# Kernel tuning notes

Measured on AMD Instinct MI355X. Metric: run time of the kernel, lower is better.

Reference implementation:

```python
import jax, jax.numpy as jnp
import numpy as np

D_IN = 1024
D_OUT = 1024
SEQ = 4096


def setup_inputs() -> dict:
    key = jax.random.key(0)
    k0, k1, k2, k3 = jax.random.split(key, 4)
    inputs = jax.random.normal(k0, (SEQ, D_IN), dtype=jnp.float32)
    # original uses torch.rand (uniform [0,1)) for weights
    W_q = jax.random.uniform(k1, (D_IN, D_OUT), dtype=jnp.float32)
    W_k = jax.random.uniform(k2, (D_IN, D_OUT), dtype=jnp.float32)
    W_v = jax.random.uniform(k3, (D_IN, D_OUT), dtype=jnp.float32)
    return {"inputs": inputs, "W_q": W_q, "W_k": W_k, "W_v": W_v}


def reference(inputs, W_q, W_k, W_v):
    queries = inputs @ W_q            # [S, d_out]
    keys = inputs @ W_k               # [S, d_out]
    values = inputs @ W_v             # [S, d_out]
    d_k = keys.shape[-1]
    scale = 1.0 / jnp.sqrt(jnp.asarray(d_k, dtype=queries.dtype))
    attn_scores = queries @ keys.T    # [S, S]
    attn_weights = jax.nn.softmax(attn_scores * scale, axis=-1)
    context_vectors = attn_weights @ values  # [S, d_out]
    return context_vectors
```

## Files before the change

### kernel.cpp

```cpp
#include <hip/hip_runtime.h>

typedef unsigned short u16;
typedef __attribute__((ext_vector_type(8))) short bf16x8;
typedef __attribute__((ext_vector_type(4))) float f32x4;

#define SEQ 4096
#define DIM 1024

__device__ __forceinline__ u16 f2bf(float f) {
  unsigned u = __float_as_uint(f);
  return (u16)((u + 0x7fffu + ((u >> 16) & 1u)) >> 16);
}
__device__ __forceinline__ float bf2f(u16 h) {
  return __uint_as_float(((unsigned)h) << 16);
}

__device__ __forceinline__ void gload_lds16(const void* g, void* l) {
  __builtin_amdgcn_global_load_lds(
      (const __attribute__((address_space(1))) void*)g,
      (__attribute__((address_space(3))) void*)l, 16, 0, 0);
}

#define VM0 asm volatile("s_waitcnt vmcnt(0)" ::: "memory")
#define VM4 asm volatile("s_waitcnt vmcnt(4)" ::: "memory")
#define VM8 asm volatile("s_waitcnt vmcnt(8)" ::: "memory")
#define BAR __builtin_amdgcn_s_barrier()

__device__ __forceinline__ size_t pkoff(int row, int col, int kd) {
  int tile = (row >> 7) * (kd >> 5) + (col >> 5);
  int r7 = row & 127, c5 = col & 31;
  int slot = ((r7 >> 4) << 6) | ((c5 >> 3) << 4) | (r7 & 15);
  return (size_t)tile * 4096 + (size_t)(slot * 8 + (c5 & 7));
}

__device__ __forceinline__ void stage_q512(const u16* __restrict__ g,
                                           int kb, int nkb, u16* ldsq, int tid) {
  const int w = tid >> 6;
  gload_lds16(g + (size_t)kb * 4096 + tid * 8, ldsq + w * 512);
  gload_lds16(g + ((size_t)nkb + kb) * 4096 + tid * 8, ldsq + 4096 + w * 512);
}

__device__ __forceinline__ void gemm3_256(
    const u16* __restrict__ A0, const u16* __restrict__ A1,
    const u16* __restrict__ B0, const u16* __restrict__ B1,
    int nkb, u16* lds, f32x4 (&acc)[8][4]) {
  const int tid = threadIdx.x;
  const int w = tid >> 6, l = tid & 63;
  const int wm = w >> 2, wn = w & 3;

#pragma unroll
  for (int mi = 0; mi < 8; ++mi)
#pragma unroll
    for (int ni = 0; ni < 4; ++ni)
      acc[mi][ni] = (f32x4){0.f, 0.f, 0.f, 0.f};

  const int QA0 = 0, QA1 = 8192, QB0 = 16384, QB1 = 24576;
  const int aoff = wm * 4096 + l * 8;
  const int boff = ((wn & 2) >> 1) * 4096 + (wn & 1) * 2048 + l * 8;

  stage_q512(A0, 0, nkb, lds + QA0, tid);
  stage_q512(B0, 0, nkb, lds + QB0, tid);
  stage_q512(B1, 0, nkb, lds + QB1, tid);
  stage_q512(A1, 0, nkb, lds + QA1, tid);

  for (int kb = 0; kb < nkb; ++kb) {
    u16* cur = lds + (kb & 1) * 32768;
    u16* nxt = lds + ((kb + 1) & 1) * 32768;
    const bool pf = (kb + 1 < nkb);
    bf16x8 a0[8], b0[4];

    VM4;
    BAR;
    if (pf) {
      stage_q512(A0, kb + 1, nkb, nxt + QA0, tid);
      stage_q512(B0, kb + 1, nkb, nxt + QB0, tid);
    }
#pragma unroll
    for (int i = 0; i < 8; ++i) a0[i] = *(const bf16x8*)(cur + QA0 + aoff + i * 512);
#pragma unroll
    for (int i = 0; i < 4; ++i) b0[i] = *(const bf16x8*)(cur + QB0 + boff + i * 512);
    __builtin_amdgcn_s_setprio(1);
#pragma unroll
    for (int mi = 0; mi < 8; ++mi)
#pragma unroll
      for (int ni = 0; ni < 4; ++ni)
        acc[mi][ni] = __builtin_amdgcn_mfma_f32_16x16x32_bf16(
            a0[mi], b0[ni], acc[mi][ni], 0, 0, 0);
    __builtin_amdgcn_s_setprio(0);

    if (pf) { VM4; } else { VM0; }
    BAR;
    if (pf) {
      stage_q512(B1, kb + 1, nkb, nxt + QB1, tid);
      stage_q512(A1, kb + 1, nkb, nxt + QA1, tid);
    }
    {
      bf16x8 b1[4];
#pragma unroll
      for (int i = 0; i < 4; ++i) b1[i] = *(const bf16x8*)(cur + QB1 + boff + i * 512);
      __builtin_amdgcn_s_setprio(1);
#pragma unroll
      for (int mi = 0; mi < 8; ++mi)
#pragma unroll
        for (int ni = 0; ni < 4; ++ni)
          acc[mi][ni] = __builtin_amdgcn_mfma_f32_16x16x32_bf16(
              a0[mi], b1[ni], acc[mi][ni], 0, 0, 0);
      __builtin_amdgcn_s_setprio(0);
    }
    {
      bf16x8 a1[8];
#pragma unroll
      for (int i = 0; i < 8; ++i) a1[i] = *(const bf16x8*)(cur + QA1 + aoff + i * 512);
      __builtin_amdgcn_s_setprio(1);
#pragma unroll
      for (int mi = 0; mi < 8; ++mi)
#pragma unroll
        for (int ni = 0; ni < 4; ++ni)
          acc[mi][ni] = __builtin_amdgcn_mfma_f32_16x16x32_bf16(
              a1[mi], b0[ni], acc[mi][ni], 0, 0, 0);
      __builtin_amdgcn_s_setprio(0);
    }
  }
  __syncthreads();
}

__device__ __forceinline__ void gemm1_256(
    const u16* __restrict__ A, const u16* __restrict__ B,
    int nkb, u16* lds, f32x4 (&acc)[8][4]) {
  const int tid = threadIdx.x;
  const int w = tid >> 6, l = tid & 63;
  const int wm = w >> 2, wn = w & 3;

#pragma unroll
  for (int mi = 0; mi < 8; ++mi)
#pragma unroll
    for (int ni = 0; ni < 4; ++ni)
      acc[mi][ni] = (f32x4){0.f, 0.f, 0.f, 0.f};

  const int aoff = wm * 4096 + l * 8;
  const int boff = ((wn & 2) >> 1) * 4096 + (wn & 1) * 2048 + l * 8;

  stage_q512(A, 0, nkb, lds + 0 * 16384, tid);
  stage_q512(B, 0, nkb, lds + 0 * 16384 + 8192, tid);
  stage_q512(A, 1, nkb, lds + 1 * 16384, tid);
  stage_q512(B, 1, nkb, lds + 1 * 16384 + 8192, tid);
  stage_q512(A, 2, nkb, lds + 2 * 16384, tid);
  stage_q512(B, 2, nkb, lds + 2 * 16384 + 8192, tid);

  for (int kb = 0; kb < nkb; ++kb) {
    if (kb + 2 < nkb) { VM8; } else if (kb + 1 < nkb) { VM4; } else { VM0; }
    BAR;
    if (kb + 3 < nkb) {
      u16* nb = lds + ((kb + 3) & 3) * 16384;
      stage_q512(A, kb + 3, nkb, nb, tid);
      stage_q512(B, kb + 3, nkb, nb + 8192, tid);
    }
    const u16* cb = lds + (kb & 3) * 16384;
    bf16x8 av[8], bv[4];
#pragma unroll
    for (int i = 0; i < 8; ++i) av[i] = *(const bf16x8*)(cb + aoff + i * 512);
#pragma unroll
    for (int i = 0; i < 4; ++i) bv[i] = *(const bf16x8*)(cb + 8192 + boff + i * 512);
    __builtin_amdgcn_s_setprio(1);
#pragma unroll
    for (int mi = 0; mi < 8; ++mi)
#pragma unroll
      for (int ni = 0; ni < 4; ++ni)
        acc[mi][ni] = __builtin_amdgcn_mfma_f32_16x16x32_bf16(
            av[mi], bv[ni], acc[mi][ni], 0, 0, 0);
    __builtin_amdgcn_s_setprio(0);
  }
  __syncthreads();
}

#define EPILOGUE_IDX                                          \
  const int tid = threadIdx.x, w = tid >> 6, l = tid & 63;    \
  const int wm = w >> 1, wn = w & 1, lr = l & 15, q = l >> 4; \
  (void)tid;

template <bool HASL>
__device__ __forceinline__ void epilogue_pack256(
    f32x4 (&acc)[8][4], u16* lds, int row0, int col0, int kd,
    u16* __restrict__ H, u16* __restrict__ L) {
  const int tid = threadIdx.x, w = tid >> 6, l = tid & 63;
  const int wm = w >> 2, wn = w & 3, lr = l & 15, q = l >> 4;
  float* lC = (float*)lds;
#pragma unroll
  for (int p = 0; p < 4; ++p) {
    if (wm == (p >> 1)) {
      const int mib = (p & 1) * 4;
#pragma unroll
      for (int mi2 = 0; mi2 < 4; ++mi2)
#pragma unroll
        for (int ni = 0; ni < 4; ++ni)
#pragma unroll
          for (int r = 0; r < 4; ++r)
            lC[(mi2 * 16 + q * 4 + r) * 260 + wn * 64 + ni * 16 + lr] =
                acc[mib + mi2][ni][r];
    }
    __syncthreads();
#pragma unroll
    for (int j = 0; j < 2; ++j) {
      int u = tid + 512 * j;
      int row = u >> 4, c0 = (u & 15) * 16;
      u16 hbuf[16], lbuf[16];
#pragma unroll
      for (int i = 0; i < 16; ++i) {
        float v = lC[row * 260 + c0 + i];
        u16 hv = f2bf(v);
        hbuf[i] = hv;
        if (HASL) lbuf[i] = f2bf(v - bf2f(hv));
      }
      int rg = row0 + p * 64 + row;
      size_t o0 = pkoff(rg, col0 + c0, kd);
      size_t o1 = pkoff(rg, col0 + c0 + 8, kd);
      *(bf16x8*)(H + o0) = *(bf16x8*)(hbuf);
      *(bf16x8*)(H + o1) = *(bf16x8*)(hbuf + 8);
      if (HASL) {
        *(bf16x8*)(L + o0) = *(bf16x8*)(lbuf);
        *(bf16x8*)(L + o1) = *(bf16x8*)(lbuf + 8);
      }
    }
    if (p < 3) __syncthreads();
  }
}


__global__ __launch_bounds__(256) void prep_kernel(
    const float* __restrict__ X,
    const float* __restrict__ W0, const float* __restrict__ W1, const float* __restrict__ W2,
    u16* __restrict__ Xh, u16* __restrict__ Xl,
    u16* __restrict__ H0, u16* __restrict__ L0,
    u16* __restrict__ H1, u16* __restrict__ L1,
    u16* __restrict__ H2) {
  const int z = blockIdx.z;
  const int tx = threadIdx.x, ty = threadIdx.y;
  if (z == 0) {
    int idx = (blockIdx.y * 32 + blockIdx.x) * 256 + ty * 32 + tx;
    int row = idx >> 6;
    int c0 = (idx & 63) * 16;
    u16 h[16], lo[16];
#pragma unroll
    for (int j = 0; j < 4; ++j) {
      float4 x = *(const float4*)(X + (size_t)row * DIM + c0 + j * 4);
      float v;
      v = x.x; h[j*4+0] = f2bf(v); lo[j*4+0] = f2bf(v - bf2f(h[j*4+0]));
      v = x.y; h[j*4+1] = f2bf(v); lo[j*4+1] = f2bf(v - bf2f(h[j*4+1]));
      v = x.z; h[j*4+2] = f2bf(v); lo[j*4+2] = f2bf(v - bf2f(h[j*4+2]));
      v = x.w; h[j*4+3] = f2bf(v); lo[j*4+3] = f2bf(v - bf2f(h[j*4+3]));
    }
    size_t o0 = pkoff(row, c0, DIM);
    size_t o1 = pkoff(row, c0 + 8, DIM);
    *(bf16x8*)(Xh + o0) = *(bf16x8*)(h);
    *(bf16x8*)(Xl + o0) = *(bf16x8*)(lo);
    *(bf16x8*)(Xh + o1) = *(bf16x8*)(h + 8);
    *(bf16x8*)(Xl + o1) = *(bf16x8*)(lo + 8);
    return;
  }
  __shared__ float t[32][33];
  const float* W = (z == 1) ? W0 : (z == 2) ? W1 : W2;
  u16* H = (z == 1) ? H0 : (z == 2) ? H1 : H2;
  u16* L = (z == 1) ? L0 : (z == 2) ? L1 : nullptr;
  const int i0 = blockIdx.y * 32, o0 = blockIdx.x * 32;
#pragma unroll
  for (int m = 0; m < 4; ++m)
    t[ty + 8 * m][tx] = W[(size_t)(i0 + ty + 8 * m) * DIM + o0 + tx];
  __syncthreads();
#pragma unroll
  for (int m = 0; m < 4; ++m) {
    float v = t[tx][ty + 8 * m];
    u16 h = f2bf(v);
    size_t o = pkoff(o0 + ty + 8 * m, i0 + tx, DIM);
    H[o] = h;
    if (L) L[o] = f2bf(v - bf2f(h));
  }
}

__global__ __launch_bounds__(512, 2) void qkv_kernel(
    const u16* __restrict__ Xh, const u16* __restrict__ Xl,
    const u16* __restrict__ Wh0, const u16* __restrict__ Wl0,
    const u16* __restrict__ Wh1, const u16* __restrict__ Wl1,
    const u16* __restrict__ Wh2,
    u16* __restrict__ Qh, u16* __restrict__ Ql,
    u16* __restrict__ Kh, u16* __restrict__ Kl,
    u16* __restrict__ VT) {
  __shared__ __align__(16) u16 lds[2 * 32768];
  const int z = blockIdx.z;
  const int bid = blockIdx.y * 4 + blockIdx.x;
  const int xcd = bid & 7, c = bid >> 3;
  const int Y = xcd * 2 + (c >> 2);
  const int Xp = c & 3;
  f32x4 acc[8][4];
  if (z < 2) {
    const u16* Wh = z ? Wh1 : Wh0;
    const u16* Wl = z ? Wl1 : Wl0;
    const int row0 = Y * 256;
    const int col0 = Xp * 256;
    gemm3_256(Xh + (size_t)row0 * DIM, Xl + (size_t)row0 * DIM,
              Wh + (size_t)col0 * DIM, Wl + (size_t)col0 * DIM,
              DIM / 32, lds, acc);
    epilogue_pack256<true>(acc, lds, row0, col0, DIM, z ? Kh : Qh, z ? Kl : Ql);
  } else {
    const int row0 = Xp * 256;
    const int col0 = Y * 256;
    gemm1_256(Wh2 + (size_t)row0 * DIM, Xh + (size_t)col0 * DIM,
              DIM / 32, lds, acc);
    epilogue_pack256<false>(acc, lds, row0, col0, SEQ, VT, nullptr);
  }
}

__global__ __launch_bounds__(512, 2) void s_kernel(
    const u16* __restrict__ Qh, const u16* __restrict__ Ql,
    const u16* __restrict__ Kh, const u16* __restrict__ Kl,
    float* __restrict__ S) {
  __shared__ __align__(16) u16 lds[2 * 32768];
  const int bid = blockIdx.y * 16 + blockIdx.x;
  const int xcd = bid & 7, c = bid >> 3;
  const int Y = (xcd & 3) * 4 + (c >> 3);
  const int X = (xcd >> 2) * 8 + (c & 7);
  const int row0 = Y * 256, col0 = X * 256;
  f32x4 acc[8][4];
  gemm3_256(Qh + (size_t)row0 * DIM, Ql + (size_t)row0 * DIM,
            Kh + (size_t)col0 * DIM, Kl + (size_t)col0 * DIM,
            DIM / 32, lds, acc);
  const int tid = threadIdx.x, w = tid >> 6, l = tid & 63;
  const int wm = w >> 2, wn = w & 3, lr = l & 15, q = l >> 4;
  const float scale = 0.03125f;
#pragma unroll
  for (int mi = 0; mi < 8; ++mi)
#pragma unroll
    for (int ni = 0; ni < 4; ++ni)
#pragma unroll
      for (int r = 0; r < 4; ++r) {
        int row = row0 + wm * 128 + mi * 16 + q * 4 + r;
        int col = col0 + wn * 64 + ni * 16 + lr;
        S[(size_t)row * SEQ + col] = acc[mi][ni][r] * scale;
      }
}

__global__ __launch_bounds__(256) void softmax_kernel(const float* __restrict__ S,
                                                      u16* __restrict__ P) {
  const int row = blockIdx.x;
  const float* s = S + (size_t)row * SEQ;
  const int tid = threadIdx.x;
  const int c0 = tid * 16;
  float v[16];
  float mx = -3.4e38f;
#pragma unroll
  for (int j = 0; j < 4; ++j) {
    float4 x = *(const float4*)(s + c0 + j * 4);
    v[j * 4 + 0] = x.x; v[j * 4 + 1] = x.y; v[j * 4 + 2] = x.z; v[j * 4 + 3] = x.w;
    mx = fmaxf(mx, fmaxf(fmaxf(x.x, x.y), fmaxf(x.z, x.w)));
  }
#pragma unroll
  for (int off = 32; off; off >>= 1) mx = fmaxf(mx, __shfl_xor(mx, off));
  __shared__ float red[8];
  const int w = tid >> 6, l = tid & 63;
  if (l == 0) red[w] = mx;
  __syncthreads();
  mx = fmaxf(fmaxf(red[0], red[1]), fmaxf(red[2], red[3]));
  float sum = 0.f;
#pragma unroll
  for (int i = 0; i < 16; ++i) {
    v[i] = __expf(v[i] - mx);
    sum += v[i];
  }
#pragma unroll
  for (int off = 32; off; off >>= 1) sum += __shfl_xor(sum, off);
  if (l == 0) red[4 + w] = sum;
  __syncthreads();
  sum = red[4] + red[5] + red[6] + red[7];
  const float inv = 1.f / sum;
  u16 p[16];
#pragma unroll
  for (int i = 0; i < 16; ++i) p[i] = f2bf(v[i] * inv);
  *(bf16x8*)(P + pkoff(row, c0, SEQ)) = *(bf16x8*)(p);
  *(bf16x8*)(P + pkoff(row, c0 + 8, SEQ)) = *(bf16x8*)(p + 8);
}


__device__ __forceinline__ void stage_tile_pk(const u16* __restrict__ g,
                                              u16* lds, int tid) {
  const int w = tid >> 6;
  gload_lds16(g + (size_t)tid * 8, lds + (size_t)(w * 64) * 8);
  gload_lds16(g + (size_t)(256 + tid) * 8, lds + (size_t)(256 + w * 64) * 8);
}

__device__ __forceinline__ void gemm1_ctd128(
    const u16* __restrict__ A, const u16* __restrict__ B,
    int nkb, u16* lds, f32x4 (&acc)[4][4]) {
  const int tid = threadIdx.x;
  const int w = tid >> 6, l = tid & 63;
  const int wm = w >> 1, wn = w & 1;

#pragma unroll
  for (int mi = 0; mi < 4; ++mi)
#pragma unroll
    for (int ni = 0; ni < 4; ++ni)
      acc[mi][ni] = (f32x4){0.f, 0.f, 0.f, 0.f};

  const int ao = wm * 2048 + l * 8;
  const int bo = wn * 2048 + l * 8;

  stage_tile_pk(A, lds + 0 * 8192, tid);
  stage_tile_pk(B, lds + 0 * 8192 + 4096, tid);
  stage_tile_pk(A + 4096, lds + 1 * 8192, tid);
  stage_tile_pk(B + 4096, lds + 1 * 8192 + 4096, tid);
  stage_tile_pk(A + 8192, lds + 2 * 8192, tid);
  stage_tile_pk(B + 8192, lds + 2 * 8192 + 4096, tid);

  for (int kb = 0; kb < nkb; ++kb) {
    if (kb + 2 < nkb) { VM8; } else if (kb + 1 < nkb) { VM4; } else { VM0; }
    BAR;
    if (kb + 3 < nkb) {
      u16* nb = lds + ((kb + 3) & 3) * 8192;
      const size_t off = (size_t)(kb + 3) * 4096;
      stage_tile_pk(A + off, nb, tid);
      stage_tile_pk(B + off, nb + 4096, tid);
    }
    const u16* cb = lds + (kb & 3) * 8192;
    bf16x8 av[4], bv[4];
#pragma unroll
    for (int i = 0; i < 4; ++i) {
      av[i] = *(const bf16x8*)(cb + ao + i * 512);
      bv[i] = *(const bf16x8*)(cb + 4096 + bo + i * 512);
    }
    __builtin_amdgcn_s_setprio(1);
#pragma unroll
    for (int mi = 0; mi < 4; ++mi)
#pragma unroll
      for (int ni = 0; ni < 4; ++ni)
        acc[mi][ni] = __builtin_amdgcn_mfma_f32_16x16x32_bf16(
            av[mi], bv[ni], acc[mi][ni], 0, 0, 0);
    __builtin_amdgcn_s_setprio(0);
  }
  __syncthreads();
}

__global__ __launch_bounds__(256, 2) void o_kernel(const u16* __restrict__ P,
                                                   const u16* __restrict__ VT,
                                                   float* __restrict__ O) {
  __shared__ __align__(16) u16 lds[4 * 8192];
  const int bid = blockIdx.y * 8 + blockIdx.x;
  const int xcd = bid & 7, c = bid >> 3;
  const int Y = xcd * 4 + (c >> 3);
  const int X = c & 7;
  const int row0 = Y * 128, col0 = X * 128;
  const u16* A = P + (size_t)row0 * SEQ;
  const u16* B = VT + (size_t)col0 * SEQ;
  f32x4 acc[4][4];
  gemm1_ctd128(A, B, 128, lds, acc);
  EPILOGUE_IDX
#pragma unroll
  for (int mi = 0; mi < 4; ++mi)
#pragma unroll
    for (int ni = 0; ni < 4; ++ni)
#pragma unroll
      for (int r = 0; r < 4; ++r) {
        int row = row0 + wm * 64 + mi * 16 + q * 4 + r;
        int col = col0 + wn * 64 + ni * 16 + lr;
        O[(size_t)row * DIM + col] = acc[mi][ni][r];
      }
}

extern "C" void kernel_launch(void* const* d_in, const int* in_sizes, int n_in,
                              void* d_out, int out_size, void* d_ws, size_t ws_size,
                              hipStream_t stream) {
  const float* X = (const float*)d_in[0];
  const float* Wq = (const float*)d_in[1];
  const float* Wk = (const float*)d_in[2];
  const float* Wv = (const float*)d_in[3];

  const size_t MB = 1024 * 1024;
  char* w = (char*)d_ws;
  u16* Xh = (u16*)(w + 0 * MB);
  u16* Xl = (u16*)(w + 8 * MB);
  u16* WqhT = (u16*)(w + 16 * MB);
  u16* WqlT = (u16*)(w + 18 * MB);
  u16* WkhT = (u16*)(w + 20 * MB);
  u16* WklT = (u16*)(w + 22 * MB);
  u16* WvhT = (u16*)(w + 24 * MB);
  u16* Qh = (u16*)(w + 26 * MB);
  u16* Ql = (u16*)(w + 34 * MB);
  u16* Kh = (u16*)(w + 42 * MB);
  u16* Kl = (u16*)(w + 50 * MB);
  u16* VT = (u16*)(w + 58 * MB);
  float* S = (float*)(w + 66 * MB);
  u16* P = (u16*)(w + 26 * MB);

  prep_kernel<<<dim3(32, 32, 4), dim3(32, 8), 0, stream>>>(
      X, Wq, Wk, Wv, Xh, Xl, WqhT, WqlT, WkhT, WklT, WvhT);
  qkv_kernel<<<dim3(DIM / 256, SEQ / 256, 3), 512, 0, stream>>>(
      Xh, Xl, WqhT, WqlT, WkhT, WklT, WvhT, Qh, Ql, Kh, Kl, VT);
  s_kernel<<<dim3(SEQ / 256, SEQ / 256), 512, 0, stream>>>(Qh, Ql, Kh, Kl, S);
  softmax_kernel<<<SEQ, 256, 0, stream>>>(S, P);
  o_kernel<<<dim3(DIM / 128, SEQ / 128), 256, 0, stream>>>(P, VT, (float*)d_out);
}
```

Measured before the change: 307.2 us.

## Software-pipeline LDS fragment reads across iterations in 512-tile GEMM

Restructures the 512-tile GEMM main loop so the A0/B0 register fragments for the next k-block are read from LDS while the current block's MFMAs run. Global-to-LDS staging of the following blocks is moved earlier, and the buffers are reused in a rotated pattern. The aim is to hide LDS read latency and barrier stalls behind MFMA work. The cost is more live registers (an extra set of A0/B0 fragments), which adds register pressure and spill risk, plus more intricate wait and barrier ordering that could race.

Measured after the change: 308.0 us. Within noise of the previous version (+0.3%).

```diff
diff --git a/kernel.cpp b/kernel.cpp
--- a/kernel.cpp
+++ b/kernel.cpp
@@ -63,62 +63,77 @@
   stage_q512(B1, 0, nkb, lds + QB1, tid);
   stage_q512(A1, 0, nkb, lds + QA1, tid);
 
+  VM4;
+  BAR;
+  bf16x8 a0c[8], b0c[4];
+#pragma unroll
+  for (int i = 0; i < 8; ++i) a0c[i] = *(const bf16x8*)(lds + QA0 + aoff + i * 512);
+#pragma unroll
+  for (int i = 0; i < 4; ++i) b0c[i] = *(const bf16x8*)(lds + QB0 + boff + i * 512);
+  stage_q512(A0, 1, nkb, lds + 32768 + QA0, tid);
+  stage_q512(B0, 1, nkb, lds + 32768 + QB0, tid);
+
   for (int kb = 0; kb < nkb; ++kb) {
     u16* cur = lds + (kb & 1) * 32768;
     u16* nxt = lds + ((kb + 1) & 1) * 32768;
     const bool pf = (kb + 1 < nkb);
-    bf16x8 a0[8], b0[4];
-
-    VM4;
-    BAR;
-    if (pf) {
-      stage_q512(A0, kb + 1, nkb, nxt + QA0, tid);
-      stage_q512(B0, kb + 1, nkb, nxt + QB0, tid);
-    }
-#pragma unroll
-    for (int i = 0; i < 8; ++i) a0[i] = *(const bf16x8*)(cur + QA0 + aoff + i * 512);
-#pragma unroll
-    for (int i = 0; i < 4; ++i) b0[i] = *(const bf16x8*)(cur + QB0 + boff + i * 512);
-    __builtin_amdgcn_s_setprio(1);
-#pragma unroll
-    for (int mi = 0; mi < 8; ++mi)
-#pragma unroll
-      for (int ni = 0; ni < 4; ++ni)
-        acc[mi][ni] = __builtin_amdgcn_mfma_f32_16x16x32_bf16(
-            a0[mi], b0[ni], acc[mi][ni], 0, 0, 0);
-    __builtin_amdgcn_s_setprio(0);
 
     if (pf) { VM4; } else { VM0; }
     BAR;
+    bf16x8 b1[4], a1[8];
+#pragma unroll
+    for (int i = 0; i < 4; ++i) b1[i] = *(const bf16x8*)(cur + QB1 + boff + i * 512);
+#pragma unroll
+    for (int i = 0; i < 8; ++i) a1[i] = *(const bf16x8*)(cur + QA1 + aoff + i * 512);
     if (pf) {
       stage_q512(B1, kb + 1, nkb, nxt + QB1, tid);
       stage_q512(A1, kb + 1, nkb, nxt + QA1, tid);
     }
-    {
-      bf16x8 b1[4];
-#pragma unroll
-      for (int i = 0; i < 4; ++i) b1[i] = *(const bf16x8*)(cur + QB1 + boff + i * 512);
-      __builtin_amdgcn_s_setprio(1);
-#pragma unroll
-      for (int mi = 0; mi < 8; ++mi)
-#pragma unroll
-        for (int ni = 0; ni < 4; ++ni)
-          acc[mi][ni] = __builtin_amdgcn_mfma_f32_16x16x32_bf16(
-              a0[mi], b1[ni], acc[mi][ni], 0, 0, 0);
-      __builtin_amdgcn_s_setprio(0);
-    }
-    {
-      bf16x8 a1[8];
-#pragma unroll
-      for (int i = 0; i < 8; ++i) a1[i] = *(const bf16x8*)(cur + QA1 + aoff + i * 512);
-      __builtin_amdgcn_s_setprio(1);
-#pragma unroll
-      for (int mi = 0; mi < 8; ++mi)
-#pragma unroll
-        for (int ni = 0; ni < 4; ++ni)
-          acc[mi][ni] = __builtin_amdgcn_mfma_f32_16x16x32_bf16(
-              a1[mi], b0[ni], acc[mi][ni], 0, 0, 0);
-      __builtin_amdgcn_s_setprio(0);
+    __builtin_amdgcn_s_setprio(1);
+#pragma unroll
+    for (int mi = 0; mi < 8; ++mi)
+#pragma unroll
+      for (int ni = 0; ni < 4; ++ni)
+        acc[mi][ni] = __builtin_amdgcn_mfma_f32_16x16x32_bf16(
+            a0c[mi], b0c[ni], acc[mi][ni], 0, 0, 0);
+    __builtin_amdgcn_s_setprio(0);
+
+    bf16x8 a0n[8], b0n[4];
+    if (pf) {
+      VM4;
+      BAR;
+#pragma unroll
+      for (int i = 0; i < 4; ++i) b0n[i] = *(const bf16x8*)(nxt + QB0 + boff + i * 512);
+      if (kb + 2 < nkb) {
+        stage_q512(A0, kb + 2, nkb, cur + QA0, tid);
+        stage_q512(B0, kb + 2, nkb, cur + QB0, tid);
+      }
+    }
+    __builtin_amdgcn_s_setprio(1);
+#pragma unroll
+    for (int mi = 0; mi < 8; ++mi)
+#pragma unroll
+      for (int ni = 0; ni < 4; ++ni)
+        acc[mi][ni] = __builtin_amdgcn_mfma_f32_16x16x32_bf16(
+            a0c[mi], b1[ni], acc[mi][ni], 0, 0, 0);
+    __builtin_amdgcn_s_setprio(0);
+    if (pf) {
+#pragma unroll
+      for (int i = 0; i < 8; ++i) a0n[i] = *(const bf16x8*)(nxt + QA0 + aoff + i * 512);
+    }
+    __builtin_amdgcn_s_setprio(1);
+#pragma unroll
+    for (int mi = 0; mi < 8; ++mi)
+#pragma unroll
+      for (int ni = 0; ni < 4; ++ni)
+        acc[mi][ni] = __builtin_amdgcn_mfma_f32_16x16x32_bf16(
+            a1[mi], b0c[ni], acc[mi][ni], 0, 0, 0);
+    __builtin_amdgcn_s_setprio(0);
+    if (pf) {
+#pragma unroll
+      for (int i = 0; i < 8; ++i) a0c[i] = a0n[i];
+#pragma unroll
+      for (int i = 0; i < 4; ++i) b0c[i] = b0n[i];
     }
   }
   __syncthreads();
```

## Fuse softmax into score GEMM epilogue with per-chunk stats and rescale in PV

Applied to the files above, without the earlier changes.

Removes the fp32 score matrix write and the separate softmax pass. The score kernel now computes a local softmax per 256-column chunk, stores unnormalized bf16 exponentials plus per-chunk max and sum, and the output GEMM rescales its accumulators at chunk boundaries using precomputed ratios, with a final normalization. This saves 64MB of fp32 traffic each way and one kernel launch. In exchange it adds rescale work inside the PV loop, lowers o_kernel occupancy via launch bounds of 1, and clamps ratios at 1e-15, which can introduce numerical error.

Result: slower. 315.4 us (+2.7%).

```diff
diff --git a/kernel.cpp b/kernel.cpp
--- a/kernel.cpp
+++ b/kernel.cpp
@@ -172,11 +172,6 @@
   }
   __syncthreads();
 }
-
-#define EPILOGUE_IDX                                          \
-  const int tid = threadIdx.x, w = tid >> 6, l = tid & 63;    \
-  const int wm = w >> 1, wn = w & 1, lr = l & 15, q = l >> 4; \
-  (void)tid;
 
 template <bool HASL>
 __device__ __forceinline__ void epilogue_pack256(
@@ -219,6 +214,63 @@
       if (HASL) {
         *(bf16x8*)(L + o0) = *(bf16x8*)(lbuf);
         *(bf16x8*)(L + o1) = *(bf16x8*)(lbuf + 8);
+      }
+    }
+    if (p < 3) __syncthreads();
+  }
+}
+
+__device__ __forceinline__ void epilogue_softmax256(
+    f32x4 (&acc)[8][4], u16* lds, int row0, int col0, int chunk,
+    u16* __restrict__ P, float* __restrict__ AuxM, float* __restrict__ AuxS) {
+  const int tid = threadIdx.x, w = tid >> 6, l = tid & 63;
+  const int wm = w >> 2, wn = w & 3, lr = l & 15, q = l >> 4;
+  const float scale = 0.03125f;
+  float* lC = (float*)lds;
+#pragma unroll
+  for (int p = 0; p < 4; ++p) {
+    if (wm == (p >> 1)) {
+      const int mib = (p & 1) * 4;
+#pragma unroll
+      for (int mi2 = 0; mi2 < 4; ++mi2)
+#pragma unroll
+        for (int ni = 0; ni < 4; ++ni)
+#pragma unroll
+          for (int r = 0; r < 4; ++r)
+            lC[(mi2 * 16 + q * 4 + r) * 260 + wn * 64 + ni * 16 + lr] =
+                acc[mib + mi2][ni][r] * scale;
+    }
+    __syncthreads();
+#pragma unroll
+    for (int j = 0; j < 2; ++j) {
+      int u = tid + 512 * j;
+      int row = u >> 4, c0 = (u & 15) * 16;
+      float v[16];
+      float mx = -3.4e38f;
+#pragma unroll
+      for (int i = 0; i < 16; ++i) {
+        v[i] = lC[row * 260 + c0 + i];
+        mx = fmaxf(mx, v[i]);
+      }
+#pragma unroll
+      for (int off = 8; off; off >>= 1) mx = fmaxf(mx, __shfl_xor(mx, off, 16));
+      float sum = 0.f;
+#pragma unroll
+      for (int i = 0; i < 16; ++i) {
+        v[i] = __expf(v[i] - mx);
+        sum += v[i];
+      }
+#pragma unroll
+      for (int off = 8; off; off >>= 1) sum += __shfl_xor(sum, off, 16);
+      u16 pb[16];
+#pragma unroll
+      for (int i = 0; i < 16; ++i) pb[i] = f2bf(v[i]);
+      int rg = row0 + p * 64 + row;
+      *(bf16x8*)(P + pkoff(rg, col0 + c0, SEQ)) = *(bf16x8*)(pb);
+      *(bf16x8*)(P + pkoff(rg, col0 + c0 + 8, SEQ)) = *(bf16x8*)(pb + 8);
+      if ((u & 15) == 0) {
+        AuxM[(size_t)rg * 16 + chunk] = mx;
+        AuxS[(size_t)rg * 16 + chunk] = sum;
       }
     }
     if (p < 3) __syncthreads();
@@ -312,7 +364,7 @@
 __global__ __launch_bounds__(512, 2) void s_kernel(
     const u16* __restrict__ Qh, const u16* __restrict__ Ql,
     const u16* __restrict__ Kh, const u16* __restrict__ Kl,
-    float* __restrict__ S) {
+    u16* __restrict__ P, float* __restrict__ AuxM, float* __restrict__ AuxS) {
   __shared__ __align__(16) u16 lds[2 * 32768];
   const int bid = blockIdx.y * 16 + blockIdx.x;
   const int xcd = bid & 7, c = bid >> 3;
@@ -323,59 +375,7 @@
   gemm3_256(Qh + (size_t)row0 * DIM, Ql + (size_t)row0 * DIM,
             Kh + (size_t)col0 * DIM, Kl + (size_t)col0 * DIM,
             DIM / 32, lds, acc);
-  const int tid = threadIdx.x, w = tid >> 6, l = tid & 63;
-  const int wm = w >> 2, wn = w & 3, lr = l & 15, q = l >> 4;
-  const float scale = 0.03125f;
-#pragma unroll
-  for (int mi = 0; mi < 8; ++mi)
-#pragma unroll
-    for (int ni = 0; ni < 4; ++ni)
-#pragma unroll
-      for (int r = 0; r < 4; ++r) {
-        int row = row0 + wm * 128 + mi * 16 + q * 4 + r;
-        int col = col0 + wn * 64 + ni * 16 + lr;
-        S[(size_t)row * SEQ + col] = acc[mi][ni][r] * scale;
-      }
-}
-
-__global__ __launch_bounds__(256) void softmax_kernel(const float* __restrict__ S,
-                                                      u16* __restrict__ P) {
-  const int row = blockIdx.x;
-  const float* s = S + (size_t)row * SEQ;
-  const int tid = threadIdx.x;
-  const int c0 = tid * 16;
-  float v[16];
-  float mx = -3.4e38f;
-#pragma unroll
-  for (int j = 0; j < 4; ++j) {
-    float4 x = *(const float4*)(s + c0 + j * 4);
-    v[j * 4 + 0] = x.x; v[j * 4 + 1] = x.y; v[j * 4 + 2] = x.z; v[j * 4 + 3] = x.w;
-    mx = fmaxf(mx, fmaxf(fmaxf(x.x, x.y), fmaxf(x.z, x.w)));
-  }
-#pragma unroll
-  for (int off = 32; off; off >>= 1) mx = fmaxf(mx, __shfl_xor(mx, off));
-  __shared__ float red[8];
-  const int w = tid >> 6, l = tid & 63;
-  if (l == 0) red[w] = mx;
-  __syncthreads();
-  mx = fmaxf(fmaxf(red[0], red[1]), fmaxf(red[2], red[3]));
-  float sum = 0.f;
-#pragma unroll
-  for (int i = 0; i < 16; ++i) {
-    v[i] = __expf(v[i] - mx);
-    sum += v[i];
-  }
-#pragma unroll
-  for (int off = 32; off; off >>= 1) sum += __shfl_xor(sum, off);
-  if (l == 0) red[4 + w] = sum;
-  __syncthreads();
-  sum = red[4] + red[5] + red[6] + red[7];
-  const float inv = 1.f / sum;
-  u16 p[16];
-#pragma unroll
-  for (int i = 0; i < 16; ++i) p[i] = f2bf(v[i] * inv);
-  *(bf16x8*)(P + pkoff(row, c0, SEQ)) = *(bf16x8*)(p);
-  *(bf16x8*)(P + pkoff(row, c0 + 8, SEQ)) = *(bf16x8*)(p + 8);
+  epilogue_softmax256(acc, lds, row0, col0, X, P, AuxM, AuxS);
 }
 
 
@@ -386,21 +386,61 @@
   gload_lds16(g + (size_t)(256 + tid) * 8, lds + (size_t)(256 + w * 64) * 8);
 }
 
-__device__ __forceinline__ void gemm1_ctd128(
-    const u16* __restrict__ A, const u16* __restrict__ B,
-    int nkb, u16* lds, f32x4 (&acc)[4][4]) {
+__global__ __launch_bounds__(256, 1) void o_kernel(
+    const u16* __restrict__ P, const u16* __restrict__ VT,
+    const float* __restrict__ AuxM, const float* __restrict__ AuxS,
+    float* __restrict__ O) {
+  __shared__ __align__(16) u16 lds[4 * 8192];
+  __shared__ float rt[128][17];
+  const int bid = blockIdx.y * 8 + blockIdx.x;
+  const int xcd = bid & 7, c = bid >> 3;
+  const int Y = xcd * 4 + (c >> 3);
+  const int X = c & 7;
+  const int row0 = Y * 128, col0 = X * 128;
   const int tid = threadIdx.x;
+
+  if (tid < 128) {
+    const int rg = row0 + tid;
+    float m[16], s[16];
+    const float4* pm = (const float4*)(AuxM + (size_t)rg * 16);
+    const float4* ps = (const float4*)(AuxS + (size_t)rg * 16);
+#pragma unroll
+    for (int i = 0; i < 4; ++i) {
+      float4 a = pm[i];
+      m[4*i] = a.x; m[4*i+1] = a.y; m[4*i+2] = a.z; m[4*i+3] = a.w;
+      float4 b = ps[i];
+      s[4*i] = b.x; s[4*i+1] = b.y; s[4*i+2] = b.z; s[4*i+3] = b.w;
+    }
+    float gmax = m[0];
+#pragma unroll
+    for (int i = 1; i < 16; ++i) gmax = fmaxf(gmax, m[i]);
+    float e[16];
+    float gsum = 0.f;
+#pragma unroll
+    for (int i = 0; i < 16; ++i) { e[i] = __expf(m[i] - gmax); gsum += e[i] * s[i]; }
+    const float inv = 1.f / gsum;
+    float b[16];
+#pragma unroll
+    for (int i = 0; i < 16; ++i) b[i] = fmaxf(e[i] * inv, 1e-15f);
+#pragma unroll
+    for (int i = 1; i < 16; ++i) rt[tid][i] = b[i - 1] / b[i];
+    rt[tid][0] = b[15];
+  }
+  __syncthreads();
+
+  const u16* A = P + (size_t)row0 * SEQ;
+  const u16* B = VT + (size_t)col0 * SEQ;
   const int w = tid >> 6, l = tid & 63;
   const int wm = w >> 1, wn = w & 1;
-
+  const int q = l >> 4, lr = l & 15;
+  const int ao = wm * 2048 + l * 8;
+  const int bo = wn * 2048 + l * 8;
+  f32x4 acc[4][4];
 #pragma unroll
   for (int mi = 0; mi < 4; ++mi)
 #pragma unroll
     for (int ni = 0; ni < 4; ++ni)
       acc[mi][ni] = (f32x4){0.f, 0.f, 0.f, 0.f};
-
-  const int ao = wm * 2048 + l * 8;
-  const int bo = wn * 2048 + l * 8;
 
   stage_tile_pk(A, lds + 0 * 8192, tid);
   stage_tile_pk(B, lds + 0 * 8192 + 4096, tid);
@@ -409,7 +449,19 @@
   stage_tile_pk(A + 8192, lds + 2 * 8192, tid);
   stage_tile_pk(B + 8192, lds + 2 * 8192 + 4096, tid);
 
+  const int nkb = 128;
   for (int kb = 0; kb < nkb; ++kb) {
+    if (kb && !(kb & 7)) {
+      const int ch = kb >> 3;
+#pragma unroll
+      for (int mi = 0; mi < 4; ++mi)
+#pragma unroll
+        for (int rr = 0; rr < 4; ++rr) {
+          const float R = rt[wm * 64 + mi * 16 + q * 4 + rr][ch];
+#pragma unroll
+          for (int ni = 0; ni < 4; ++ni) acc[mi][ni][rr] *= R;
+        }
+    }
     if (kb + 2 < nkb) { VM8; } else if (kb + 1 < nkb) { VM4; } else { VM0; }
     BAR;
     if (kb + 3 < nkb) {
@@ -434,33 +486,20 @@
             av[mi], bv[ni], acc[mi][ni], 0, 0, 0);
     __builtin_amdgcn_s_setprio(0);
   }
-  __syncthreads();
-}
-
-__global__ __launch_bounds__(256, 2) void o_kernel(const u16* __restrict__ P,
-                                                   const u16* __restrict__ VT,
-                                                   float* __restrict__ O) {
-  __shared__ __align__(16) u16 lds[4 * 8192];
-  const int bid = blockIdx.y * 8 + blockIdx.x;
-  const int xcd = bid & 7, c = bid >> 3;
-  const int Y = xcd * 4 + (c >> 3);
-  const int X = c & 7;
-  const int row0 = Y * 128, col0 = X * 128;
-  const u16* A = P + (size_t)row0 * SEQ;
-  const u16* B = VT + (size_t)col0 * SEQ;
-  f32x4 acc[4][4];
-  gemm1_ctd128(A, B, 128, lds, acc);
-  EPILOGUE_IDX
+
 #pragma unroll
   for (int mi = 0; mi < 4; ++mi)
 #pragma unroll
-    for (int ni = 0; ni < 4; ++ni)
-#pragma unroll
-      for (int r = 0; r < 4; ++r) {
-        int row = row0 + wm * 64 + mi * 16 + q * 4 + r;
-        int col = col0 + wn * 64 + ni * 16 + lr;
-        O[(size_t)row * DIM + col] = acc[mi][ni][r];
+    for (int rr = 0; rr < 4; ++rr) {
+      const int rloc = wm * 64 + mi * 16 + q * 4 + rr;
+      const float F = rt[rloc][0];
+      const int row = row0 + rloc;
+#pragma unroll
+      for (int ni = 0; ni < 4; ++ni) {
+        const int col = col0 + wn * 64 + ni * 16 + lr;
+        O[(size_t)row * DIM + col] = acc[mi][ni][rr] * F;
       }
+    }
 }
 
 extern "C" void kernel_launch(void* const* d_in, const int* in_sizes, int n_in,
@@ -485,14 +524,16 @@
   u16* Kh = (u16*)(w + 42 * MB);
   u16* Kl = (u16*)(w + 50 * MB);
   u16* VT = (u16*)(w + 58 * MB);
-  float* S = (float*)(w + 66 * MB);
-  u16* P = (u16*)(w + 26 * MB);
+  u16* P = (u16*)(w + 66 * MB);
+  float* AuxM = (float*)(w + 98 * MB);
+  float* AuxS = (float*)(w + 99 * MB);
 
   prep_kernel<<<dim3(32, 32, 4), dim3(32, 8), 0, stream>>>(
       X, Wq, Wk, Wv, Xh, Xl, WqhT, WqlT, WkhT, WklT, WvhT);
   qkv_kernel<<<dim3(DIM / 256, SEQ / 256, 3), 512, 0, stream>>>(
       Xh, Xl, WqhT, WqlT, WkhT, WklT, WvhT, Qh, Ql, Kh, Kl, VT);
-  s_kernel<<<dim3(SEQ / 256, SEQ / 256), 512, 0, stream>>>(Qh, Ql, Kh, Kl, S);
-  softmax_kernel<<<SEQ, 256, 0, stream>>>(S, P);
-  o_kernel<<<dim3(DIM / 128, SEQ / 128), 256, 0, stream>>>(P, VT, (float*)d_out);
-}
+  s_kernel<<<dim3(SEQ / 256, SEQ / 256), 512, 0, stream>>>(
+      Qh, Ql, Kh, Kl, P, AuxM, AuxS);
+  o_kernel<<<dim3(DIM / 128, SEQ / 128), 256, 0, stream>>>(
+      P, VT, AuxM, AuxS, (float*)d_out);
+}
```
